# Optimization experiments

Hardware: AMD Instinct MI355X
Metric: run time of the kernel (lower is better)

## Reference

```python
import jax, jax.numpy as jnp
import numpy as np

B, NPG, EPG = 512, 64, 256          # graphs, nodes/graph, edges/graph
N, E = B * NPG, B * EPG             # 32768 nodes, 131072 edges
FN, FE, FG = 128, 64, 64            # node / edge / global feature dims
MH, MD = 512, 256                   # message MLP hidden, message dim
UH, UD = 512, 256                   # update MLP hidden, node embedding dim
GD, AD = 128, 8                     # group embedding dim, action dim


def _lin_init(key, fan_in, fan_out):
    kw, kb = jax.random.split(key)
    s = 1.0 / np.sqrt(fan_in)
    W = jax.random.uniform(kw, (fan_in, fan_out), minval=-s, maxval=s)
    b = jax.random.uniform(kb, (fan_out,), minval=-s, maxval=s)
    return W, b


def setup_inputs() -> dict:
    key = jax.random.key(0)
    ks = jax.random.split(key, 16)
    nodes = jax.random.normal(ks[0], (N, FN), dtype=jnp.float32)
    edge_attr = jax.random.normal(ks[1], (E, FE), dtype=jnp.float32)
    global_attr = jax.random.normal(ks[2], (B, FG), dtype=jnp.float32)
    # per-graph structured connectivity (edges stay within their graph)
    edge_graph_id = jnp.repeat(jnp.arange(B), EPG)
    src_index = edge_graph_id * NPG + jax.random.randint(ks[3], (E,), 0, NPG)
    target_index = edge_graph_id * NPG + jax.random.randint(ks[4], (E,), 0, NPG)
    batch_indices = jnp.repeat(jnp.arange(B), NPG)
    target_batch_wide = jnp.arange(B) * NPG + jax.random.randint(ks[5], (B,), 0, NPG)
    # parameters (Linear weights stored as (in, out))
    W_m0, b_m0 = _lin_init(ks[6], 2 * FN + FE + FG, MH)
    W_m1, b_m1 = _lin_init(ks[7], MH, MD)
    W_u0, b_u0 = _lin_init(ks[8], MD + FN + FG, UH)
    W_u1, b_u1 = _lin_init(ks[9], UH, UD)
    W_g, b_g = _lin_init(ks[10], UD + FG, GD)
    W_a, b_a = _lin_init(ks[11], UD + GD, AD)
    return dict(nodes=nodes, edge_attr=edge_attr, global_attr=global_attr,
                src_index=src_index, target_index=target_index,
                edge_graph_id=edge_graph_id, batch_indices=batch_indices,
                target_batch_wide=target_batch_wide,
                W_m0=W_m0, b_m0=b_m0, W_m1=W_m1, b_m1=b_m1,
                W_u0=W_u0, b_u0=b_u0, W_u1=W_u1, b_u1=b_u1,
                W_g=W_g, b_g=b_g, W_a=W_a, b_a=b_a)


def _mlp2(x, W0, b0, W1, b1):
    # Sequential(Lin,ReLU,Lin,ReLU) as built in __init__
    h = jax.nn.relu(x @ W0 + b0)
    return jax.nn.relu(h @ W1 + b1)


def _scatter_max0(x, idx, num_segments):
    # torch_scatter.scatter_max fills empty segments with 0; inputs here are
    # ReLU outputs (>= 0) so clamping segment_max at 0 reproduces it exactly.
    return jnp.maximum(jax.ops.segment_max(x, idx, num_segments=num_segments), 0.0)


def reference(nodes, edge_attr, global_attr, src_index, target_index,
              edge_graph_id, batch_indices, target_batch_wide,
              W_m0, b_m0, W_m1, b_m1, W_u0, b_u0, W_u1, b_u1,
              W_g, b_g, W_a, b_a):
    # message phase: gather -> concat -> MLP
    tmp = jnp.concatenate([nodes[src_index], edge_attr, nodes[target_index],
                           global_attr[edge_graph_id]], axis=1)      # [E, 2FN+FE+FG]
    message = jax.nn.relu(_mlp2(tmp, W_m0, b_m0, W_m1, b_m1))        # [E, MD]
    # scatter-max aggregate messages onto target nodes
    aggr = _scatter_max0(message, target_index, N)                   # [N, MD]
    # node update
    upd_in = jnp.concatenate([nodes, aggr, global_attr[batch_indices]], axis=1)
    upd = _mlp2(upd_in, W_u0, b_u0, W_u1, b_u1)                      # [N, UD]
    # graph-level pooling + global update
    agg_nodes = _scatter_max0(upd, batch_indices, B)                 # [B, UD]
    group = jax.nn.relu(jnp.concatenate([agg_nodes, global_attr], axis=1) @ W_g + b_g)
    # action head on chosen node per graph
    chosen = upd[target_batch_wide]                                  # [B, UD]
    logits = jnp.concatenate([chosen, group], axis=1) @ W_a + b_a    # [B, AD]
    return jax.nn.softmax(logits, axis=1)
```

## Files before the change

### kernel.cpp

```cpp
#include <hip/hip_runtime.h>
#include <hip/hip_bf16.h>

typedef __bf16 bf16x8 __attribute__((ext_vector_type(8)));
typedef float f32x4 __attribute__((ext_vector_type(4)));

#define MFMA_BF16(A, B, C) __builtin_amdgcn_mfma_f32_16x16x32_bf16((A), (B), (C), 0, 0, 0)

namespace cfg {
constexpr int NB = 512;
constexpr int NPG = 64;
constexpr int EPG = 256;
constexpr int FN = 128, FE = 64, FG = 64;
constexpr int XP  = 2 * FN + FE + FG;
constexpr int XPP = XP + 8;
constexpr int HPP = 256 + 8;
constexpr int X2P  = FN + 256 + FG;
constexpr int X2PP = X2P + 8;
constexpr int OFF_XS1 = 0;
constexpr int OFF_HS1 = 64 * XPP * 2;
constexpr int OFF_X2  = 0;
constexpr int OFF_US  = 0;
constexpr int OFF_AG  = 64 * XPP * 2 + 64 * HPP * 2;
constexpr int OFF_HS2 = OFF_AG;
constexpr int OFF_TL  = OFF_AG + 64 * 256 * 4;
constexpr int OFF_PS  = OFF_TL + 256;
constexpr int OFF_GS  = OFF_PS + 1024;
constexpr int OFF_LS  = OFF_GS + 512;
constexpr int LDS_TOTAL = OFF_LS + 32;
}

__device__ __forceinline__ ushort f2bf(float f) {
  union { float f; unsigned u; } x; x.f = f;
  unsigned r = x.u + 0x7FFFu + ((x.u >> 16) & 1u);
  return (ushort)(r >> 16);
}
__device__ __forceinline__ float bf2f(ushort u) {
  union { unsigned u; float f; } x; x.u = ((unsigned)u) << 16; return x.f;
}
__device__ __forceinline__ void cvt8(const float* __restrict__ s, ushort* d) {
  float4 a = *(const float4*)s, b = *(const float4*)(s + 4);
  d[0] = f2bf(a.x); d[1] = f2bf(a.y); d[2] = f2bf(a.z); d[3] = f2bf(a.w);
  d[4] = f2bf(b.x); d[5] = f2bf(b.y); d[6] = f2bf(b.z); d[7] = f2bf(b.w);
}

__global__ void ktrans_cvt(const float* __restrict__ in, ushort* __restrict__ out,
                           int R, int C) {
  __shared__ float t[32][33];
  const int c0 = blockIdx.x * 32, r0 = blockIdx.y * 32;
  const int tx = threadIdx.x & 31, ty = threadIdx.x >> 5;
#pragma unroll
  for (int i = 0; i < 32; i += 8) {
    int r = r0 + ty + i, c = c0 + tx;
    t[ty + i][tx] = (r < R && c < C) ? in[(size_t)r * C + c] : 0.f;
  }
  __syncthreads();
#pragma unroll
  for (int i = 0; i < 32; i += 8) {
    int c = c0 + ty + i, r = r0 + tx;
    if (c < C && r < R) out[(size_t)c * R + r] = f2bf(t[tx][ty + i]);
  }
}

__launch_bounds__(512, 2)
__global__ void k_fused(const float* __restrict__ nodes,
                        const float* __restrict__ eattr,
                        const float* __restrict__ glob,
                        const int* __restrict__ srci,
                        const int* __restrict__ tgti,
                        const int* __restrict__ tbw,
                        const ushort* __restrict__ WTm0,
                        const float* __restrict__ bm0,
                        const ushort* __restrict__ WTm1,
                        const float* __restrict__ bm1,
                        const ushort* __restrict__ WTu0,
                        const float* __restrict__ bu0,
                        const ushort* __restrict__ WTu1,
                        const float* __restrict__ bu1,
                        const ushort* __restrict__ WTg,
                        const float* __restrict__ bg,
                        const ushort* __restrict__ WTa,
                        const float* __restrict__ ba,
                        float* __restrict__ out)
{
  using namespace cfg;
  extern __shared__ __align__(16) char smem[];
  ushort*   Xs1 = (ushort*)(smem + OFF_XS1);
  ushort*   Hs1 = (ushort*)(smem + OFF_HS1);
  ushort*   X2  = (ushort*)(smem + OFF_X2);
  ushort*   Us  = (ushort*)(smem + OFF_US);
  unsigned* Ag  = (unsigned*)(smem + OFF_AG);
  ushort*   Hs2 = (ushort*)(smem + OFF_HS2);
  int*      tl  = (int*)(smem + OFF_TL);
  float*    Ps  = (float*)(smem + OFF_PS);
  float*    Gs  = (float*)(smem + OFF_GS);
  float*    Ls  = (float*)(smem + OFF_LS);

  const int g    = blockIdx.x;
  const int tid  = threadIdx.x;
  const int lane = tid & 63;
  const int wv   = tid >> 6;
  const int l16  = lane & 15;
  const int l4   = lane >> 4;

  for (int i = tid; i < 64 * 256; i += 512) Ag[i] = 0u;

  for (int t = 0; t < 4; ++t) {
    const int e0 = g * EPG + t * 64;
    __syncthreads();
    if (tid < 64) tl[tid] = tgti[e0 + tid] - g * NPG;
    for (int li = tid; li < 64 * 48; li += 512) {
      int r = li / 48, c = li % 48;
      int e = e0 + r;
      const float* src;
      if (c < 16)       src = nodes + (size_t)srci[e] * FN + c * 8;
      else if (c < 24)  src = eattr + (size_t)e * FE + (c - 16) * 8;
      else if (c < 40)  src = nodes + (size_t)tgti[e] * FN + (c - 24) * 8;
      else              src = glob + (size_t)g * FG + (c - 40) * 8;
      alignas(16) ushort tmp[8];
      cvt8(src, tmp);
      *(uint4*)(Xs1 + r * XPP + c * 8) = *(const uint4*)tmp;
    }
    __syncthreads();

    f32x4 acc2[4][2] = {};

    for (int h = 0; h < 2; ++h) {
      f32x4 acc1[4][2] = {};
#pragma unroll 2
      for (int k = 0; k < XP; k += 32) {
        bf16x8 af[4], bw[2];
#pragma unroll
        for (int m = 0; m < 4; ++m)
          af[m] = *(const bf16x8*)(Xs1 + (m * 16 + l16) * XPP + k + 8 * l4);
#pragma unroll
        for (int n = 0; n < 2; ++n) {
          int nc = h * 256 + wv * 32 + n * 16 + l16;
          bw[n] = *(const bf16x8*)(WTm0 + (size_t)nc * XP + k + 8 * l4);
        }
#pragma unroll
        for (int m = 0; m < 4; ++m)
#pragma unroll
          for (int n = 0; n < 2; ++n)
            acc1[m][n] = MFMA_BF16(af[m], bw[n], acc1[m][n]);
      }
      __syncthreads();
#pragma unroll
      for (int n = 0; n < 2; ++n) {
        int col = wv * 32 + n * 16 + l16;
        float bb = bm0[h * 256 + col];
#pragma unroll
        for (int m = 0; m < 4; ++m)
#pragma unroll
          for (int j = 0; j < 4; ++j) {
            float v = acc1[m][n][j] + bb;
            Hs1[(m * 16 + l4 * 4 + j) * HPP + col] = f2bf(v > 0.f ? v : 0.f);
          }
      }
      __syncthreads();
#pragma unroll 2
      for (int k = 0; k < 256; k += 32) {
        bf16x8 af[4], bw[2];
#pragma unroll
        for (int m = 0; m < 4; ++m)
          af[m] = *(const bf16x8*)(Hs1 + (m * 16 + l16) * HPP + k + 8 * l4);
#pragma unroll
        for (int n = 0; n < 2; ++n) {
          int nc = wv * 32 + n * 16 + l16;
          bw[n] = *(const bf16x8*)(WTm1 + (size_t)nc * 512 + h * 256 + k + 8 * l4);
        }
#pragma unroll
        for (int m = 0; m < 4; ++m)
#pragma unroll
          for (int n = 0; n < 2; ++n)
            acc2[m][n] = MFMA_BF16(af[m], bw[n], acc2[m][n]);
      }
    }
#pragma unroll
    for (int n = 0; n < 2; ++n) {
      int col = wv * 32 + n * 16 + l16;
      float bb = bm1[col];
#pragma unroll
      for (int m = 0; m < 4; ++m)
#pragma unroll
        for (int j = 0; j < 4; ++j) {
          float v = acc2[m][n][j] + bb;
          if (v > 0.f) {
            int row = m * 16 + l4 * 4 + j;
            atomicMax(&Ag[tl[row] * 256 + col], __float_as_uint(v));
          }
        }
    }
  }
  __syncthreads();

  for (int li = tid; li < 64 * 56; li += 512) {
    int r = li / 56, c = li % 56;
    alignas(16) ushort tmp[8];
    if (c >= 16 && c < 48) {
      const unsigned* a = Ag + r * 256 + (c - 16) * 8;
#pragma unroll
      for (int j = 0; j < 8; ++j) tmp[j] = f2bf(__uint_as_float(a[j]));
    } else {
      const float* src = (c < 16) ? nodes + (size_t)(g * 64 + r) * FN + c * 8
                                  : glob + (size_t)g * FG + (c - 48) * 8;
      cvt8(src, tmp);
    }
    *(uint4*)(X2 + r * X2PP + c * 8) = *(const uint4*)tmp;
  }
  __syncthreads();

  {
    f32x4 acc2u[4][2] = {};
    for (int h = 0; h < 2; ++h) {
      f32x4 acc1[4][2] = {};
#pragma unroll 2
      for (int k = 0; k < X2P; k += 32) {
        bf16x8 af[4], bw[2];
#pragma unroll
        for (int m = 0; m < 4; ++m)
          af[m] = *(const bf16x8*)(X2 + (m * 16 + l16) * X2PP + k + 8 * l4);
#pragma unroll
        for (int n = 0; n < 2; ++n) {
          int nc = h * 256 + wv * 32 + n * 16 + l16;
          bw[n] = *(const bf16x8*)(WTu0 + (size_t)nc * X2P + k + 8 * l4);
        }
#pragma unroll
        for (int m = 0; m < 4; ++m)
#pragma unroll
          for (int n = 0; n < 2; ++n)
            acc1[m][n] = MFMA_BF16(af[m], bw[n], acc1[m][n]);
      }
      __syncthreads();
#pragma unroll
      for (int n = 0; n < 2; ++n) {
        int col = wv * 32 + n * 16 + l16;
        float bb = bu0[h * 256 + col];
#pragma unroll
        for (int m = 0; m < 4; ++m)
#pragma unroll
          for (int j = 0; j < 4; ++j) {
            float v = acc1[m][n][j] + bb;
            Hs2[(m * 16 + l4 * 4 + j) * HPP + col] = f2bf(v > 0.f ? v : 0.f);
          }
      }
      __syncthreads();
#pragma unroll 2
      for (int k = 0; k < 256; k += 32) {
        bf16x8 af[4], bw[2];
#pragma unroll
        for (int m = 0; m < 4; ++m)
          af[m] = *(const bf16x8*)(Hs2 + (m * 16 + l16) * HPP + k + 8 * l4);
#pragma unroll
        for (int n = 0; n < 2; ++n) {
          int nc = wv * 32 + n * 16 + l16;
          bw[n] = *(const bf16x8*)(WTu1 + (size_t)nc * 512 + h * 256 + k + 8 * l4);
        }
#pragma unroll
        for (int m = 0; m < 4; ++m)
#pragma unroll
          for (int n = 0; n < 2; ++n)
            acc2u[m][n] = MFMA_BF16(af[m], bw[n], acc2u[m][n]);
      }
    }
#pragma unroll
    for (int n = 0; n < 2; ++n) {
      int col = wv * 32 + n * 16 + l16;
      float bb = bu1[col];
#pragma unroll
      for (int m = 0; m < 4; ++m)
#pragma unroll
        for (int j = 0; j < 4; ++j) {
          float v = acc2u[m][n][j] + bb;
          Us[(m * 16 + l4 * 4 + j) * HPP + col] = f2bf(v > 0.f ? v : 0.f);
        }
    }
  }
  __syncthreads();

  if (tid < 256) {
    float mx = 0.f;
    for (int r = 0; r < 64; ++r) mx = fmaxf(mx, bf2f(Us[r * HPP + tid]));
    Ps[tid] = mx;
  }
  __syncthreads();

  for (int jj = 0; jj < 16; ++jj) {
    int j = wv * 16 + jj;
    const ushort* wr = WTg + (size_t)j * 320;
    float part = 0.f;
    for (int k = lane; k < 320; k += 64) {
      float x = (k < 256) ? Ps[k] : glob[(size_t)g * FG + (k - 256)];
      part += x * bf2f(wr[k]);
    }
#pragma unroll
    for (int o = 32; o > 0; o >>= 1) part += __shfl_down(part, o);
    if (lane == 0) {
      float v = part + bg[j];
      Gs[j] = v > 0.f ? v : 0.f;
    }
  }
  __syncthreads();

  {
    const int tb = tbw[g] - g * 64;
    const ushort* wr = WTa + (size_t)wv * 384;
    float part = 0.f;
    for (int k = lane; k < 384; k += 64) {
      float x = (k < 256) ? bf2f(Us[tb * HPP + k]) : Gs[k - 256];
      part += x * bf2f(wr[k]);
    }
#pragma unroll
    for (int o = 32; o > 0; o >>= 1) part += __shfl_down(part, o);
    if (lane == 0) Ls[wv] = part + ba[wv];
  }
  __syncthreads();

  if (tid == 0) {
    float mx = Ls[0];
#pragma unroll
    for (int i = 1; i < 8; ++i) mx = fmaxf(mx, Ls[i]);
    float e[8], sum = 0.f;
#pragma unroll
    for (int i = 0; i < 8; ++i) { e[i] = __expf(Ls[i] - mx); sum += e[i]; }
    float inv = 1.f / sum;
#pragma unroll
    for (int i = 0; i < 8; ++i) out[(size_t)g * 8 + i] = e[i] * inv;
  }
}

extern "C" void kernel_launch(void* const* d_in, const int* in_sizes, int n_in,
                              void* d_out, int out_size, void* d_ws, size_t ws_size,
                              hipStream_t stream) {
  (void)in_sizes; (void)n_in; (void)out_size; (void)ws_size;
  using namespace cfg;
  const float* nodes = (const float*)d_in[0];
  const float* eattr = (const float*)d_in[1];
  const float* glob  = (const float*)d_in[2];
  const int* srci = (const int*)d_in[3];
  const int* tgti = (const int*)d_in[4];
  const int* tbw  = (const int*)d_in[7];
  const float* W_m0 = (const float*)d_in[8];
  const float* b_m0 = (const float*)d_in[9];
  const float* W_m1 = (const float*)d_in[10];
  const float* b_m1 = (const float*)d_in[11];
  const float* W_u0 = (const float*)d_in[12];
  const float* b_u0 = (const float*)d_in[13];
  const float* W_u1 = (const float*)d_in[14];
  const float* b_u1 = (const float*)d_in[15];
  const float* W_g  = (const float*)d_in[16];
  const float* b_g  = (const float*)d_in[17];
  const float* W_a  = (const float*)d_in[18];
  const float* b_a  = (const float*)d_in[19];

  char* ws = (char*)d_ws;
  size_t off = 0;
  auto alloc = [&](size_t bytes) {
    char* p = ws + off; off += (bytes + 255) & ~(size_t)255; return p;
  };
  ushort* WTm0 = (ushort*)alloc((size_t)512 * 384 * 2);
  ushort* WTm1 = (ushort*)alloc((size_t)256 * 512 * 2);
  ushort* WTu0 = (ushort*)alloc((size_t)512 * 448 * 2);
  ushort* WTu1 = (ushort*)alloc((size_t)256 * 512 * 2);
  ushort* WTg  = (ushort*)alloc((size_t)128 * 320 * 2);
  ushort* WTa  = (ushort*)alloc((size_t)8 * 384 * 2);

  dim3 tb(256);
  auto T = [&](const float* in, ushort* outp, int R, int C) {
    ktrans_cvt<<<dim3((C + 31) / 32, (R + 31) / 32), tb, 0, stream>>>(in, outp, R, C);
  };
  T(W_m0, WTm0, 384, 512);
  T(W_m1, WTm1, 512, 256);
  T(W_u0, WTu0, 448, 512);
  T(W_u1, WTu1, 512, 256);
  T(W_g,  WTg,  320, 128);
  T(W_a,  WTa,  384, 8);

  hipFuncSetAttribute((const void*)k_fused, hipFuncAttributeMaxDynamicSharedMemorySize,
                      (int)LDS_TOTAL);
  k_fused<<<NB, 512, LDS_TOTAL, stream>>>(nodes, eattr, glob, srci, tgti, tbw,
                                          WTm0, b_m0, WTm1, b_m1,
                                          WTu0, b_u0, WTu1, b_u1,
                                          WTg, b_g, WTa, b_a, (float*)d_out);
}
```

Measured before the change: 348.7 us.

## Use 1024-thread blocks with one column tile per wave and prefetch edge tiles

Doubles the block to 16 waves, so each wave computes a single 16-column slice of every GEMM instead of two. This halves per-wave accumulator registers and work. The gather of the next 64-edge tile is issued into registers before the current tile's MLP runs, overlapping global loads with MFMA compute. In exchange there is more per-block barrier cost, the same A-fragment LDS reads are repeated across twice as many waves, and the prefetch registers add pressure under the tighter launch bound.

```diff
diff --git a/kernel.cpp b/kernel.cpp
--- a/kernel.cpp
+++ b/kernel.cpp
@@ -61,7 +61,7 @@
   }
 }
 
-__launch_bounds__(512, 2)
+__launch_bounds__(1024, 4)
 __global__ void k_fused(const float* __restrict__ nodes,
                         const float* __restrict__ eattr,
                         const float* __restrict__ glob,
@@ -101,89 +101,96 @@
   const int wv   = tid >> 6;
   const int l16  = lane & 15;
   const int l4   = lane >> 4;
-
-  for (int i = tid; i < 64 * 256; i += 512) Ag[i] = 0u;
-
-  for (int t = 0; t < 4; ++t) {
-    const int e0 = g * EPG + t * 64;
-    __syncthreads();
-    if (tid < 64) tl[tid] = tgti[e0 + tid] - g * NPG;
-    for (int li = tid; li < 64 * 48; li += 512) {
+  const int col  = wv * 16 + l16;
+
+  for (int i = tid; i < 64 * 256; i += 1024) Ag[i] = 0u;
+
+  float4 pa[3], pb[3]; int ptl = 0;
+  auto load_tile = [&](int t) {
+    const int e0g = g * EPG + t * 64;
+#pragma unroll
+    for (int i = 0; i < 3; ++i) {
+      int li = tid + i * 1024;
       int r = li / 48, c = li % 48;
-      int e = e0 + r;
+      int e = e0g + r;
       const float* src;
       if (c < 16)       src = nodes + (size_t)srci[e] * FN + c * 8;
       else if (c < 24)  src = eattr + (size_t)e * FE + (c - 16) * 8;
       else if (c < 40)  src = nodes + (size_t)tgti[e] * FN + (c - 24) * 8;
       else              src = glob + (size_t)g * FG + (c - 40) * 8;
+      pa[i] = *(const float4*)src;
+      pb[i] = *(const float4*)(src + 4);
+    }
+    if (tid < 64) ptl = tgti[e0g + tid] - g * NPG;
+  };
+  auto store_tile = [&]() {
+#pragma unroll
+    for (int i = 0; i < 3; ++i) {
+      int li = tid + i * 1024;
+      int r = li / 48, c = li % 48;
       alignas(16) ushort tmp[8];
-      cvt8(src, tmp);
+      tmp[0] = f2bf(pa[i].x); tmp[1] = f2bf(pa[i].y);
+      tmp[2] = f2bf(pa[i].z); tmp[3] = f2bf(pa[i].w);
+      tmp[4] = f2bf(pb[i].x); tmp[5] = f2bf(pb[i].y);
+      tmp[6] = f2bf(pb[i].z); tmp[7] = f2bf(pb[i].w);
       *(uint4*)(Xs1 + r * XPP + c * 8) = *(const uint4*)tmp;
     }
+    if (tid < 64) tl[tid] = ptl;
+  };
+
+  load_tile(0);
+  for (int t = 0; t < 4; ++t) {
     __syncthreads();
-
-    f32x4 acc2[4][2] = {};
+    store_tile();
+    if (t < 3) load_tile(t + 1);
+    __syncthreads();
+
+    f32x4 acc2[4] = {};
 
     for (int h = 0; h < 2; ++h) {
-      f32x4 acc1[4][2] = {};
+      f32x4 acc1[4] = {};
 #pragma unroll 2
       for (int k = 0; k < XP; k += 32) {
-        bf16x8 af[4], bw[2];
+        bf16x8 af[4], bw;
 #pragma unroll
         for (int m = 0; m < 4; ++m)
           af[m] = *(const bf16x8*)(Xs1 + (m * 16 + l16) * XPP + k + 8 * l4);
-#pragma unroll
-        for (int n = 0; n < 2; ++n) {
-          int nc = h * 256 + wv * 32 + n * 16 + l16;
-          bw[n] = *(const bf16x8*)(WTm0 + (size_t)nc * XP + k + 8 * l4);
-        }
-#pragma unroll
-        for (int m = 0; m < 4; ++m)
-#pragma unroll
-          for (int n = 0; n < 2; ++n)
-            acc1[m][n] = MFMA_BF16(af[m], bw[n], acc1[m][n]);
+        bw = *(const bf16x8*)(WTm0 + (size_t)(h * 256 + col) * XP + k + 8 * l4);
+#pragma unroll
+        for (int m = 0; m < 4; ++m)
+          acc1[m] = MFMA_BF16(af[m], bw, acc1[m]);
       }
       __syncthreads();
-#pragma unroll
-      for (int n = 0; n < 2; ++n) {
-        int col = wv * 32 + n * 16 + l16;
+      {
         float bb = bm0[h * 256 + col];
 #pragma unroll
         for (int m = 0; m < 4; ++m)
 #pragma unroll
           for (int j = 0; j < 4; ++j) {
-            float v = acc1[m][n][j] + bb;
+            float v = acc1[m][j] + bb;
             Hs1[(m * 16 + l4 * 4 + j) * HPP + col] = f2bf(v > 0.f ? v : 0.f);
           }
       }
       __syncthreads();
 #pragma unroll 2
       for (int k = 0; k < 256; k += 32) {
-        bf16x8 af[4], bw[2];
+        bf16x8 af[4], bw;
 #pragma unroll
         for (int m = 0; m < 4; ++m)
           af[m] = *(const bf16x8*)(Hs1 + (m * 16 + l16) * HPP + k + 8 * l4);
-#pragma unroll
-        for (int n = 0; n < 2; ++n) {
-          int nc = wv * 32 + n * 16 + l16;
-          bw[n] = *(const bf16x8*)(WTm1 + (size_t)nc * 512 + h * 256 + k + 8 * l4);
-        }
-#pragma unroll
-        for (int m = 0; m < 4; ++m)
-#pragma unroll
-          for (int n = 0; n < 2; ++n)
-            acc2[m][n] = MFMA_BF16(af[m], bw[n], acc2[m][n]);
-      }
-    }
-#pragma unroll
-    for (int n = 0; n < 2; ++n) {
-      int col = wv * 32 + n * 16 + l16;
+        bw = *(const bf16x8*)(WTm1 + (size_t)col * 512 + h * 256 + k + 8 * l4);
+#pragma unroll
+        for (int m = 0; m < 4; ++m)
+          acc2[m] = MFMA_BF16(af[m], bw, acc2[m]);
+      }
+    }
+    {
       float bb = bm1[col];
 #pragma unroll
       for (int m = 0; m < 4; ++m)
 #pragma unroll
         for (int j = 0; j < 4; ++j) {
-          float v = acc2[m][n][j] + bb;
+          float v = acc2[m][j] + bb;
           if (v > 0.f) {
             int row = m * 16 + l4 * 4 + j;
             atomicMax(&Ag[tl[row] * 256 + col], __float_as_uint(v));
@@ -193,7 +200,7 @@
   }
   __syncthreads();
 
-  for (int li = tid; li < 64 * 56; li += 512) {
+  for (int li = tid; li < 64 * 56; li += 1024) {
     int r = li / 56, c = li % 56;
     alignas(16) ushort tmp[8];
     if (c >= 16 && c < 48) {
@@ -210,67 +217,51 @@
   __syncthreads();
 
   {
-    f32x4 acc2u[4][2] = {};
+    f32x4 acc2u[4] = {};
     for (int h = 0; h < 2; ++h) {
-      f32x4 acc1[4][2] = {};
+      f32x4 acc1[4] = {};
 #pragma unroll 2
       for (int k = 0; k < X2P; k += 32) {
-        bf16x8 af[4], bw[2];
+        bf16x8 af[4], bw;
 #pragma unroll
         for (int m = 0; m < 4; ++m)
           af[m] = *(const bf16x8*)(X2 + (m * 16 + l16) * X2PP + k + 8 * l4);
-#pragma unroll
-        for (int n = 0; n < 2; ++n) {
-          int nc = h * 256 + wv * 32 + n * 16 + l16;
-          bw[n] = *(const bf16x8*)(WTu0 + (size_t)nc * X2P + k + 8 * l4);
-        }
-#pragma unroll
-        for (int m = 0; m < 4; ++m)
-#pragma unroll
-          for (int n = 0; n < 2; ++n)
-            acc1[m][n] = MFMA_BF16(af[m], bw[n], acc1[m][n]);
+        bw = *(const bf16x8*)(WTu0 + (size_t)(h * 256 + col) * X2P + k + 8 * l4);
+#pragma unroll
+        for (int m = 0; m < 4; ++m)
+          acc1[m] = MFMA_BF16(af[m], bw, acc1[m]);
       }
       __syncthreads();
-#pragma unroll
-      for (int n = 0; n < 2; ++n) {
-        int col = wv * 32 + n * 16 + l16;
+      {
         float bb = bu0[h * 256 + col];
 #pragma unroll
         for (int m = 0; m < 4; ++m)
 #pragma unroll
           for (int j = 0; j < 4; ++j) {
-            float v = acc1[m][n][j] + bb;
+            float v = acc1[m][j] + bb;
             Hs2[(m * 16 + l4 * 4 + j) * HPP + col] = f2bf(v > 0.f ? v : 0.f);
           }
       }
       __syncthreads();
 #pragma unroll 2
       for (int k = 0; k < 256; k += 32) {
-        bf16x8 af[4], bw[2];
+        bf16x8 af[4], bw;
 #pragma unroll
         for (int m = 0; m < 4; ++m)
           af[m] = *(const bf16x8*)(Hs2 + (m * 16 + l16) * HPP + k + 8 * l4);
-#pragma unroll
-        for (int n = 0; n < 2; ++n) {
-          int nc = wv * 32 + n * 16 + l16;
-          bw[n] = *(const bf16x8*)(WTu1 + (size_t)nc * 512 + h * 256 + k + 8 * l4);
-        }
-#pragma unroll
-        for (int m = 0; m < 4; ++m)
-#pragma unroll
-          for (int n = 0; n < 2; ++n)
-            acc2u[m][n] = MFMA_BF16(af[m], bw[n], acc2u[m][n]);
-      }
-    }
-#pragma unroll
-    for (int n = 0; n < 2; ++n) {
-      int col = wv * 32 + n * 16 + l16;
+        bw = *(const bf16x8*)(WTu1 + (size_t)col * 512 + h * 256 + k + 8 * l4);
+#pragma unroll
+        for (int m = 0; m < 4; ++m)
+          acc2u[m] = MFMA_BF16(af[m], bw, acc2u[m]);
+      }
+    }
+    {
       float bb = bu1[col];
 #pragma unroll
       for (int m = 0; m < 4; ++m)
 #pragma unroll
         for (int j = 0; j < 4; ++j) {
-          float v = acc2u[m][n][j] + bb;
+          float v = acc2u[m][j] + bb;
           Us[(m * 16 + l4 * 4 + j) * HPP + col] = f2bf(v > 0.f ? v : 0.f);
         }
     }
@@ -284,8 +275,8 @@
   }
   __syncthreads();
 
-  for (int jj = 0; jj < 16; ++jj) {
-    int j = wv * 16 + jj;
+  for (int jj = 0; jj < 8; ++jj) {
+    int j = wv * 8 + jj;
     const ushort* wr = WTg + (size_t)j * 320;
     float part = 0.f;
     for (int k = lane; k < 320; k += 64) {
@@ -301,7 +292,7 @@
   }
   __syncthreads();
 
-  {
+  if (wv < 8) {
     const int tb = tbw[g] - g * 64;
     const ushort* wr = WTa + (size_t)wv * 384;
     float part = 0.f;
@@ -377,8 +368,8 @@
 
   hipFuncSetAttribute((const void*)k_fused, hipFuncAttributeMaxDynamicSharedMemorySize,
                       (int)LDS_TOTAL);
-  k_fused<<<NB, 512, LDS_TOTAL, stream>>>(nodes, eattr, glob, srci, tgti, tbw,
-                                          WTm0, b_m0, WTm1, b_m1,
-                                          WTu0, b_u0, WTu1, b_u1,
-                                          WTg, b_g, WTa, b_a, (float*)d_out);
-}
+  k_fused<<<NB, 1024, LDS_TOTAL, stream>>>(nodes, eattr, glob, srci, tgti, tbw,
+                                           WTm0, b_m0, WTm1, b_m1,
+                                           WTu0, b_u0, WTu1, b_u1,
+                                           WTg, b_g, WTa, b_a, (float*)d_out);
+}
```

After: 297.0 us. 14.8% less time.
